# Kernel tuning notes

Measured on AMD Instinct MI355X. Metric: run time of the kernel, lower is better.

Reference implementation:

```python
import jax, jax.numpy as jnp
import numpy as np
import math

B, S, D, H = 2, 2048, 512, 8
DH = D // H  # 64

def setup_inputs() -> dict:
    key = jax.random.key(0)
    ks = jax.random.split(key, 7)
    x = jax.random.normal(ks[0], (B, S, D), jnp.float32)
    shift = jax.random.normal(ks[1], (B, S, S), jnp.float32)
    mask = jax.random.randint(ks[2], (B, S, S), 0, 2).astype(jnp.float32)
    W = jax.random.normal(ks[3], (3 * D, D), jnp.float32) / math.sqrt(D)
    b = jnp.zeros((3 * D,), jnp.float32)
    Wo = jax.random.normal(ks[4], (D, D), jnp.float32) / math.sqrt(D)
    bo = jnp.zeros((D,), jnp.float32)
    return {"x": x, "shift": shift, "mask": mask, "W": W, "b": b, "Wo": Wo, "bo": bo}

def reference(x, shift, mask, W, b, Wo, bo):
    # qkv projection: (B,S,3D). torch chunk(n_heads) then chunk(3) =>
    # per-head layout is [q_h | k_h | v_h] within each 3*DH-sized slice.
    qkv = x @ W.T + b
    qkv = qkv.reshape(B, S, H, 3, DH)
    qkv = jnp.moveaxis(qkv, (2, 3), (0, 1))  # (H, 3, B, S, DH)
    q, k, v = qkv[:, 0], qkv[:, 1], qkv[:, 2]  # each (H, B, S, DH)

    head_scale = jnp.exp2(-jnp.arange(H, dtype=jnp.float32)).reshape(H, 1, 1, 1)  # 2^-h
    logits = jnp.einsum('hbqd,hbkd->hbqk', q, k) / math.sqrt(DH)
    logits = logits - head_scale * shift[None]          # ALiBi-style per-head shift
    m = mask[None]                                       # (1,B,S,S)
    logits = logits * m - 1e8 * (1.0 - m)
    att = jax.nn.softmax(logits, axis=-1)
    o = jnp.einsum('hbqk,hbkd->hbqd', att, v)            # (H,B,S,DH)
    o = jnp.moveaxis(o, 0, 2).reshape(B, S, D)           # concat heads on last dim
    return o @ Wo.T + bo
```

## Files before the change

### kernel.cpp

```cpp
#include <hip/hip_runtime.h>
#include <math.h>

constexpr int Bc = 2, Sc = 2048, Dc = 512, Hc = 8, DHc = 64;
constexpr int NQKV = 3 * Dc;

typedef unsigned short u16;
typedef unsigned int u32;
typedef __attribute__((ext_vector_type(8))) __bf16 bf16x8;
typedef __attribute__((ext_vector_type(16))) float f32x16;

#define MFMA32 __builtin_amdgcn_mfma_f32_32x32x16_bf16

__device__ inline uint2 splitpack2(float a, float b) {
  u32 ua = __float_as_uint(a), ub = __float_as_uint(b);
  u32 hi = (ub & 0xFFFF0000u) | (ua >> 16);
  float ra = a - __uint_as_float(ua & 0xFFFF0000u);
  float rb = b - __uint_as_float(ub & 0xFFFF0000u);
  u32 lo = (__float_as_uint(rb) & 0xFFFF0000u) | (__float_as_uint(ra) >> 16);
  return uint2{hi, lo};
}
__device__ inline void split1(float v, u16& hi, u16& lo) {
  u32 u = __float_as_uint(v);
  hi = (u16)(u >> 16);
  float r = v - __uint_as_float(u & 0xFFFF0000u);
  lo = (u16)(__float_as_uint(r) >> 16);
}

__global__ __launch_bounds__(256) void presplit_xw(
    const float* __restrict__ x, const float* __restrict__ W,
    u16* __restrict__ Xhi, u16* __restrict__ Xlo, u16* __restrict__ Whi,
    u16* __restrict__ Wlo) {
  const u32 g = blockIdx.x * 256 + threadIdx.x;
  const float* src;
  u16 *dh, *dl;
  if (g < 262144u) {
    src = x + (size_t)g * 8;
    dh = Xhi + (size_t)g * 8;
    dl = Xlo + (size_t)g * 8;
  } else {
    const u32 gw = g - 262144u;
    src = W + (size_t)gw * 8;
    dh = Whi + (size_t)gw * 8;
    dl = Wlo + (size_t)gw * 8;
  }
  const float4 v0 = *(const float4*)src;
  const float4 v1 = *(const float4*)(src + 4);
  const uint2 p0 = splitpack2(v0.x, v0.y), p1 = splitpack2(v0.z, v0.w);
  const uint2 p2 = splitpack2(v1.x, v1.y), p3 = splitpack2(v1.z, v1.w);
  *(uint4*)dh = uint4{p0.x, p1.x, p2.x, p3.x};
  *(uint4*)dl = uint4{p0.y, p1.y, p2.y, p3.y};
}

__global__ __launch_bounds__(256) void presplit_wo(const float* __restrict__ Wo,
                                                   u16* __restrict__ Wohi,
                                                   u16* __restrict__ Wolo) {
  const u32 g = blockIdx.x * 256 + threadIdx.x;
  const float* src = Wo + (size_t)g * 8;
  const float4 v0 = *(const float4*)src;
  const float4 v1 = *(const float4*)(src + 4);
  const uint2 p0 = splitpack2(v0.x, v0.y), p1 = splitpack2(v0.z, v0.w);
  const uint2 p2 = splitpack2(v1.x, v1.y), p3 = splitpack2(v1.z, v1.w);
  *(uint4*)(Wohi + (size_t)g * 8) = uint4{p0.x, p1.x, p2.x, p3.x};
  *(uint4*)(Wolo + (size_t)g * 8) = uint4{p0.y, p1.y, p2.y, p3.y};
}

#define G1_ISSUE(K0)                          \
  {                                           \
    a0h = *(const uint4*)(srcA0h + (K0));     \
    a0l = *(const uint4*)(srcA0l + (K0));     \
    a1h = *(const uint4*)(srcA1h + (K0));     \
    a1l = *(const uint4*)(srcA1l + (K0));     \
    b0h = *(const uint4*)(srcBh + (K0));      \
    b0l = *(const uint4*)(srcBl + (K0));      \
  }
#define G1_COMMIT()                           \
  {                                           \
    *(uint4*)dA0h = a0h;                      \
    *(uint4*)dA0l = a0l;                      \
    *(uint4*)dA1h = a1h;                      \
    *(uint4*)dA1l = a1l;                      \
    *(uint4*)dBh = b0h;                       \
    *(uint4*)dBl = b0l;                       \
  }

__global__ __launch_bounds__(256, 3) void gemm1_mfma(
    const u16* __restrict__ Xhi, const u16* __restrict__ Xlo,
    const u16* __restrict__ Whi, const u16* __restrict__ Wlo,
    const float* __restrict__ bias, u16* __restrict__ Qhi,
    u16* __restrict__ Qlo, u16* __restrict__ Khi, u16* __restrict__ Klo,
    u16* __restrict__ Vthi, u16* __restrict__ Vtlo) {
  __shared__ __align__(16) u16 pool[18432];
  const int tid = threadIdx.x;
  const int wave = tid >> 6, lane = tid & 63, l31 = lane & 31, lhi = lane >> 5;
  const int wm = wave >> 1, wn = wave & 1;
  const int m0 = blockIdx.y * 128, n0 = blockIdx.x * 64;

  const int mA = tid >> 2, kgA = tid & 3;
  const int rowA = (kgA & 1) * 32 + (mA & 31);
  u16* const dA0h = &pool[(((mA >> 5) * 2 + (kgA >> 1)) * 64 + rowA) * 8];
  u16* const dA0l = dA0h + 4096;
  u16* const dA1h =
      &pool[(((2 + (mA >> 5)) * 2 + (kgA >> 1)) * 64 + rowA) * 8];
  u16* const dA1l = dA1h + 4096;
  u16* const dBh = &pool[8192 + (((mA >> 5) * 2 + (kgA >> 1)) * 64 + rowA) * 8];
  u16* const dBl = dBh + 2048;
  const u16* const srcA0h = Xhi + (size_t)(m0 + mA) * 512 + kgA * 8;
  const u16* const srcA0l = Xlo + (size_t)(m0 + mA) * 512 + kgA * 8;
  const u16* const srcA1h = srcA0h + 64 * 512;
  const u16* const srcA1l = srcA0l + 64 * 512;
  const u16* const srcBh = Whi + (size_t)(n0 + mA) * 512 + kgA * 8;
  const u16* const srcBl = Wlo + (size_t)(n0 + mA) * 512 + kgA * 8;

  f32x16 acc[2];
#pragma unroll
  for (int r = 0; r < 16; ++r) {
    acc[0][r] = 0.f;
    acc[1][r] = 0.f;
  }

  uint4 a0h, a0l, a1h, a1l, b0h, b0l;
  G1_ISSUE(0);
  for (int k0 = 0; k0 < 512; k0 += 32) {
    G1_COMMIT();
    __syncthreads();
    if (k0 < 480) G1_ISSUE(k0 + 32);
#pragma unroll
    for (int t = 0; t < 2; ++t) {
      const bf16x8 bh =
          *(const bf16x8*)&pool[8192 + (((0 * 2 + wn) * 2 + t) * 64 + lane) * 8];
      const bf16x8 bl =
          *(const bf16x8*)&pool[8192 + (((1 * 2 + wn) * 2 + t) * 64 + lane) * 8];
#pragma unroll
      for (int ti = 0; ti < 2; ++ti) {
        const bf16x8 ah =
            *(const bf16x8*)&pool[(((0 * 4 + wm * 2 + ti) * 2 + t) * 64 + lane) * 8];
        const bf16x8 al =
            *(const bf16x8*)&pool[(((1 * 4 + wm * 2 + ti) * 2 + t) * 64 + lane) * 8];
        acc[ti] = MFMA32(ah, bh, acc[ti], 0, 0, 0);
        acc[ti] = MFMA32(ah, bl, acc[ti], 0, 0, 0);
        acc[ti] = MFMA32(al, bh, acc[ti], 0, 0, 0);
      }
    }
    __syncthreads();
  }

  const int n = n0 + wn * 32 + l31;
  const float bn = bias[n];
  const int h = n0 / 192;
  const int t3 = (n0 % 192) / 64;
  const int dh = wn * 32 + l31;
  const int batch = m0 >> 11;
  const int s0 = m0 & 2047;
  const int hbq = h * 2 + batch;

#pragma unroll
  for (int ti = 0; ti < 2; ++ti)
#pragma unroll
    for (int r = 0; r < 16; ++r) {
      const int tl = wm * 64 + ti * 32 + (r & 3) + 8 * (r >> 2) + 4 * lhi;
      float val = acc[ti][r] + bn;
      if (t3 == 0) val *= 0.125f;
      u16 hi, lo;
      split1(val, hi, lo);
      pool[tl * 72 + dh] = hi;
      pool[9216 + tl * 72 + dh] = lo;
    }
  __syncthreads();

  u16 *d0, *d1;
  if (t3 == 0) {
    d0 = Qhi;
    d1 = Qlo;
  } else if (t3 == 1) {
    d0 = Khi;
    d1 = Klo;
  } else {
    d0 = Vthi;
    d1 = Vtlo;
  }

  if (t3 != 2) {
    const size_t base = ((size_t)hbq * 2048 + s0) * 64;
#pragma unroll
    for (int p = 0; p < 2; ++p) {
      u16* dst = (p ? d1 : d0) + base;
#pragma unroll
      for (int j = 0; j < 4; ++j) {
        const int g = tid * 32 + j * 8;
        const int token = g >> 6, dh8 = g & 63;
        *(uint4*)(dst + g) = *(const uint4*)&pool[p * 9216 + token * 72 + dh8];
      }
    }
  } else {
    const int d = tid >> 2, tp = (tid & 3) * 32;
#pragma unroll
    for (int p = 0; p < 2; ++p) {
      u16* dst = (p ? d1 : d0) + ((size_t)hbq * 64 + d) * 2048 + s0 + tp;
      u32 w[16];
#pragma unroll
      for (int j = 0; j < 16; ++j) {
        const u16 a = pool[p * 9216 + (tp + 2 * j) * 72 + d];
        const u16 b2 = pool[p * 9216 + (tp + 2 * j + 1) * 72 + d];
        w[j] = (u32)a | ((u32)b2 << 16);
      }
#pragma unroll
      for (int j = 0; j < 4; ++j)
        *(uint4*)(dst + j * 8) =
            uint4{w[4 * j], w[4 * j + 1], w[4 * j + 2], w[4 * j + 3]};
    }
  }
}

constexpr int KF0 = 8320;
constexpr int VF0 = 16512;
constexpr int PF0 = 24704;

#define ISSUE_TILE(KT)                                   \
  {                                                      \
    const float* sp_ = shr + (KT);                       \
    const float* mp_ = mkr + (KT);                       \
    pS0 = *(const float4*)(sp_);                         \
    pS1 = *(const float4*)(sp_ + 4);                     \
    pS2 = *(const float4*)(sp_ + 8);                     \
    pS3 = *(const float4*)(sp_ + 12);                    \
    pM0 = *(const float4*)(mp_);                         \
    pM1 = *(const float4*)(mp_ + 4);                     \
    pM2 = *(const float4*)(mp_ + 8);                     \
    pM3 = *(const float4*)(mp_ + 12);                    \
    const u16* h_ = kvsrc_hi + (size_t)(KT) * ktmul;     \
    const u16* l_ = kvsrc_lo + (size_t)(KT) * ktmul;     \
    pK0 = *(const uint4*)(h_);                           \
    pK1 = *(const uint4*)(l_);                           \
    pK2 = *(const uint4*)(h_ + 8);                       \
    pK3 = *(const uint4*)(l_ + 8);                       \
    pK4 = *(const uint4*)(h_ + 16);                      \
    pK5 = *(const uint4*)(l_ + 16);                      \
    pK6 = *(const uint4*)(h_ + 24);                      \
    pK7 = *(const uint4*)(l_ + 24);                      \
  }

#define COMMIT_TILE()                                    \
  {                                                      \
    smd[0 * 65] = (pM0.x != 0.f) ? pS0.x : 1e13f;        \
    smd[1 * 65] = (pM0.y != 0.f) ? pS0.y : 1e13f;        \
    smd[2 * 65] = (pM0.z != 0.f) ? pS0.z : 1e13f;        \
    smd[3 * 65] = (pM0.w != 0.f) ? pS0.w : 1e13f;        \
    smd[4 * 65] = (pM1.x != 0.f) ? pS1.x : 1e13f;        \
    smd[5 * 65] = (pM1.y != 0.f) ? pS1.y : 1e13f;        \
    smd[6 * 65] = (pM1.z != 0.f) ? pS1.z : 1e13f;        \
    smd[7 * 65] = (pM1.w != 0.f) ? pS1.w : 1e13f;        \
    smd[8 * 65] = (pM2.x != 0.f) ? pS2.x : 1e13f;        \
    smd[9 * 65] = (pM2.y != 0.f) ? pS2.y : 1e13f;        \
    smd[10 * 65] = (pM2.z != 0.f) ? pS2.z : 1e13f;       \
    smd[11 * 65] = (pM2.w != 0.f) ? pS2.w : 1e13f;       \
    smd[12 * 65] = (pM3.x != 0.f) ? pS3.x : 1e13f;       \
    smd[13 * 65] = (pM3.y != 0.f) ? pS3.y : 1e13f;       \
    smd[14 * 65] = (pM3.z != 0.f) ? pS3.z : 1e13f;       \
    smd[15 * 65] = (pM3.w != 0.f) ? pS3.w : 1e13f;       \
    *(uint4*)(kvdst + 0) = pK0;                          \
    *(uint4*)(kvdst + 4096) = pK1;                       \
    *(uint4*)(kvdst + 256) = pK2;                        \
    *(uint4*)(kvdst + 4096 + 256) = pK3;                 \
    *(uint4*)(kvdst + 512) = pK4;                        \
    *(uint4*)(kvdst + 4096 + 512) = pK5;                 \
    *(uint4*)(kvdst + 768) = pK6;                        \
    *(uint4*)(kvdst + 4096 + 768) = pK7;                 \
  }

__global__ __launch_bounds__(256, 2) void attn_mfma(
    const u16* __restrict__ Qhi, const u16* __restrict__ Qlo,
    const u16* __restrict__ Khi, const u16* __restrict__ Klo,
    const u16* __restrict__ Vthi, const u16* __restrict__ Vtlo,
    const float* __restrict__ shift, const float* __restrict__ mask,
    u16* __restrict__ Othi, u16* __restrict__ Otlo) {
  const int head = blockIdx.z, b = blockIdx.y, qb = blockIdx.x;
  const int tid = threadIdx.x;
  const int wave = tid >> 6;
  const int wq = wave >> 1, wk = wave & 1;
  const int lane = tid & 63;
  const int l31 = lane & 31, lhi = lane >> 5;

  __shared__ __align__(16) u16 smem[32896];
  float* SMs = (float*)smem;
  u16* Pw = smem + PF0 + wave * 2048;

  const size_t hb = (size_t)head * Bc + b;
  const int ql = wq * 32 + l31;
  const int qg = qb * 64 + ql;

  bf16x8 qf[2][4];
  {
    const size_t qbase = (hb * Sc + qg) * DHc;
#pragma unroll
    for (int t = 0; t < 4; ++t) {
      qf[0][t] = *(const bf16x8*)(Qhi + qbase + t * 16 + lhi * 8);
      qf[1][t] = *(const bf16x8*)(Qlo + qbase + t * 16 + lhi * 8);
    }
  }
  const float hs = exp2f(-(float)head);

  const int smq = tid >> 2, smk = (tid & 3) * 16;
  const float* shr = shift + ((size_t)b * Sc + qb * 64 + smq) * Sc + smk;
  const float* mkr = mask + ((size_t)b * Sc + qb * 64 + smq) * Sc + smk;
  float* const smd = SMs + (size_t)smk * 65 + smq;

  const int kr = lane >> 1, kh2 = lane & 1;
  const size_t kfix = (hb * Sc + wk * 32 + kr) * 64 + kh2 * 32;
  const size_t vfix = (hb * 64 + lane) * 2048 + wk * 32;
  const int vmt = lane >> 5, vdl = lane & 31;

  const u16* const kvsrc_hi = (wq == 0) ? (Khi + kfix) : (Vthi + vfix);
  const u16* const kvsrc_lo = (wq == 0) ? (Klo + kfix) : (Vtlo + vfix);
  const int ktmul = (wq == 0) ? 64 : 1;
  u16* const kvdst = (wq == 0)
                         ? &smem[KF0 + (wk * 4 + kh2 * 2) * 512 + kr * 8]
                         : &smem[VF0 + (wk * 4 + vmt * 2) * 512 + vdl * 8];

  float m_run = -INFINITY, l_run = 0.f;
  f32x16 o0, o1;
#pragma unroll
  for (int i = 0; i < 16; ++i) {
    o0[i] = 0.f;
    o1[i] = 0.f;
  }

  float4 pS0, pS1, pS2, pS3, pM0, pM1, pM2, pM3;
  uint4 pK0, pK1, pK2, pK3, pK4, pK5, pK6, pK7;

  ISSUE_TILE(0);
  for (int it = 0; it < 32; ++it) {
    COMMIT_TILE();
    __syncthreads();
    if (it < 31) ISSUE_TILE(it * 64 + 64);

    f32x16 s;
#pragma unroll
    for (int i = 0; i < 16; ++i) s[i] = 0.f;
    __builtin_amdgcn_s_setprio(1);
#pragma unroll
    for (int t = 0; t < 4; ++t) {
      const bf16x8 kh = *(const bf16x8*)&smem[KF0 +
          (((0 * 2 + wk) * 4 + t) * 64 + lane) * 8];
      const bf16x8 kl = *(const bf16x8*)&smem[KF0 +
          (((1 * 2 + wk) * 4 + t) * 64 + lane) * 8];
      s = MFMA32(kh, qf[0][t], s, 0, 0, 0);
      s = MFMA32(kh, qf[1][t], s, 0, 0, 0);
      s = MFMA32(kl, qf[0][t], s, 0, 0, 0);
    }
    __builtin_amdgcn_s_setprio(0);

    float p[16];
    float kmax = -INFINITY;
#pragma unroll
    for (int c = 0; c < 4; ++c) {
#pragma unroll
      for (int e = 0; e < 4; ++e) {
        const int kl_ = wk * 32 + c * 8 + lhi * 4 + e;
        const float a = hs * SMs[(size_t)kl_ * 65 + ql];
        const float lg = s[4 * c + e] - a;
        p[4 * c + e] = lg;
        kmax = fmaxf(kmax, lg);
      }
    }
    kmax = fmaxf(kmax, __shfl_xor(kmax, 32, 64));
    const float mnew = fmaxf(m_run, kmax);
    const float alpha = __expf(m_run - mnew);
    float rsum = 0.f;
#pragma unroll
    for (int r = 0; r < 16; ++r) {
      p[r] = __expf(p[r] - mnew);
      rsum += p[r];
    }
    rsum += __shfl_xor(rsum, 32, 64);
    l_run = l_run * alpha + rsum;
    m_run = mnew;
#pragma unroll
    for (int i = 0; i < 16; ++i) {
      o0[i] *= alpha;
      o1[i] *= alpha;
    }

#pragma unroll
    for (int c = 0; c < 4; ++c) {
      const uint2 s01 = splitpack2(p[4 * c + 0], p[4 * c + 1]);
      const uint2 s23 = splitpack2(p[4 * c + 2], p[4 * c + 3]);
      const int t = c >> 1, lh = c & 1;
      const int bi = (t * 64 + lh * 32 + l31) * 8 + lhi * 4;
      *(uint2*)&Pw[bi] = uint2{s01.x, s23.x};
      *(uint2*)&Pw[1024 + bi] = uint2{s01.y, s23.y};
    }

    __builtin_amdgcn_s_setprio(1);
#pragma unroll
    for (int t = 0; t < 2; ++t) {
      const bf16x8 ph = *(const bf16x8*)&Pw[(t * 64 + lane) * 8];
      const bf16x8 pl_ = *(const bf16x8*)&Pw[1024 + (t * 64 + lane) * 8];
      bf16x8 vh = *(const bf16x8*)&smem[VF0 +
          ((((0 * 2 + wk) * 2 + 0) * 2 + t) * 64 + lane) * 8];
      bf16x8 vl = *(const bf16x8*)&smem[VF0 +
          ((((1 * 2 + wk) * 2 + 0) * 2 + t) * 64 + lane) * 8];
      o0 = MFMA32(vh, ph, o0, 0, 0, 0);
      o0 = MFMA32(vh, pl_, o0, 0, 0, 0);
      o0 = MFMA32(vl, ph, o0, 0, 0, 0);
      vh = *(const bf16x8*)&smem[VF0 +
          ((((0 * 2 + wk) * 2 + 1) * 2 + t) * 64 + lane) * 8];
      vl = *(const bf16x8*)&smem[VF0 +
          ((((1 * 2 + wk) * 2 + 1) * 2 + t) * 64 + lane) * 8];
      o1 = MFMA32(vh, ph, o1, 0, 0, 0);
      o1 = MFMA32(vh, pl_, o1, 0, 0, 0);
      o1 = MFMA32(vl, ph, o1, 0, 0, 0);
    }
    __builtin_amdgcn_s_setprio(0);
    __syncthreads();
  }

  float* mL = (float*)(smem + KF0);
  float* lL = mL + 64;
  float* Om = lL + 64;
  if (wk == 1) {
    if (lhi == 0) {
      mL[wq * 32 + l31] = m_run;
      lL[wq * 32 + l31] = l_run;
    }
#pragma unroll
    for (int mt = 0; mt < 2; ++mt)
#pragma unroll
      for (int r = 0; r < 16; ++r) {
        const int row = mt * 32 + (r & 3) + 8 * (r >> 2) + 4 * lhi;
        Om[(wq * 64 + row) * 33 + l31] = (mt ? o1[r] : o0[r]);
      }
  }
  __syncthreads();
  if (wk == 0) {
    const float m1 = mL[wq * 32 + l31];
    const float l1v = lL[wq * 32 + l31];
    const float mst = fmaxf(m_run, m1);
    const float a0 = __expf(m_run - mst), a1 = __expf(m1 - mst);
    const float inv = 1.f / (a0 * l_run + a1 * l1v);
    const int tok = b * 2048 + qg;
#pragma unroll
    for (int mt = 0; mt < 2; ++mt)
#pragma unroll
      for (int r = 0; r < 16; ++r) {
        const int row = mt * 32 + (r & 3) + 8 * (r >> 2) + 4 * lhi;
        const float val = (a0 * (mt ? o1[r] : o0[r]) +
                           a1 * Om[(wq * 64 + row) * 33 + l31]) *
                          inv;
        const int d = head * 64 + row;
        u16 hi, lo;
        split1(val, hi, lo);
        const size_t idx = ((size_t)(d >> 3) * 4096 + tok) * 8 + (d & 7);
        Othi[idx] = hi;
        Otlo[idx] = lo;
      }
  }
}

#define G2_ISSUE(K0)                                        \
  {                                                         \
    g2ah = *(const uint4*)(srcAh + (size_t)(K0) * 4096);    \
    g2al = *(const uint4*)(srcAl + (size_t)(K0) * 4096);    \
    g2bh = *(const uint4*)(srcBh + (K0));                   \
    g2bl = *(const uint4*)(srcBl + (K0));                   \
  }
#define G2_COMMIT()                                         \
  {                                                         \
    *(uint4*)dAh = g2ah;                                    \
    *(uint4*)dAl = g2al;                                    \
    *(uint4*)dBh = g2bh;                                    \
    *(uint4*)dBl = g2bl;                                    \
  }

__global__ __launch_bounds__(256, 2) void gemm2_mfma(
    const u16* __restrict__ Othi, const u16* __restrict__ Otlo,
    const u16* __restrict__ Wohi, const u16* __restrict__ Wolo,
    const float* __restrict__ bo, float* __restrict__ out) {
  __shared__ __align__(16) u16 Af[2][2][2][64][8];
  __shared__ __align__(16) u16 Bf[2][2][2][64][8];
  const int tid = threadIdx.x;
  const int wave = tid >> 6, lane = tid & 63, l31 = lane & 31, lhi = lane >> 5;
  const int wm = wave >> 1, wn = wave & 1;
  const int m0 = blockIdx.y * 64, n0 = blockIdx.x * 64;

  const int cA = tid >> 6, tokA = tid & 63;
  u16* const dAh = &Af[0][tokA >> 5][cA >> 1][(cA & 1) * 32 + (tokA & 31)][0];
  u16* const dAl = &Af[1][tokA >> 5][cA >> 1][(cA & 1) * 32 + (tokA & 31)][0];
  const u16* const srcAh = Othi + ((size_t)cA * 4096 + m0 + tokA) * 8;
  const u16* const srcAl = Otlo + ((size_t)cA * 4096 + m0 + tokA) * 8;
  const int nB = tid >> 2, cB = tid & 3;
  u16* const dBh = &Bf[0][nB >> 5][cB >> 1][(cB & 1) * 32 + (nB & 31)][0];
  u16* const dBl = &Bf[1][nB >> 5][cB >> 1][(cB & 1) * 32 + (nB & 31)][0];
  const u16* const srcBh = Wohi + (size_t)(n0 + nB) * 512 + cB * 8;
  const u16* const srcBl = Wolo + (size_t)(n0 + nB) * 512 + cB * 8;

  f32x16 acc;
#pragma unroll
  for (int r = 0; r < 16; ++r) acc[r] = 0.f;

  uint4 g2ah, g2al, g2bh, g2bl;
  G2_ISSUE(0);
  for (int k0 = 0; k0 < 512; k0 += 32) {
    G2_COMMIT();
    __syncthreads();
    if (k0 < 480) G2_ISSUE(k0 + 32);
#pragma unroll
    for (int t = 0; t < 2; ++t) {
      const bf16x8 ah = *(const bf16x8*)&Af[0][wm][t][lane][0];
      const bf16x8 al = *(const bf16x8*)&Af[1][wm][t][lane][0];
      const bf16x8 bh = *(const bf16x8*)&Bf[0][wn][t][lane][0];
      const bf16x8 bl = *(const bf16x8*)&Bf[1][wn][t][lane][0];
      acc = MFMA32(ah, bh, acc, 0, 0, 0);
      acc = MFMA32(ah, bl, acc, 0, 0, 0);
      acc = MFMA32(al, bh, acc, 0, 0, 0);
    }
    __syncthreads();
  }

  const int n = n0 + wn * 32 + l31;
  const float bn = bo[n];
#pragma unroll
  for (int r = 0; r < 16; ++r) {
    const int m = m0 + wm * 32 + (r & 3) + 8 * (r >> 2) + 4 * lhi;
    out[(size_t)m * 512 + n] = acc[r] + bn;
  }
}

extern "C" void kernel_launch(void* const* d_in, const int* in_sizes, int n_in,
                              void* d_out, int out_size, void* d_ws,
                              size_t ws_size, hipStream_t stream) {
  const float* x = (const float*)d_in[0];
  const float* shift = (const float*)d_in[1];
  const float* mask = (const float*)d_in[2];
  const float* W = (const float*)d_in[3];
  const float* b = (const float*)d_in[4];
  const float* Wo = (const float*)d_in[5];
  const float* bo = (const float*)d_in[6];
  float* out = (float*)d_out;

  const size_t P = (size_t)Hc * Bc * Sc * DHc;
  u16* ws0 = (u16*)d_ws;
  u16* Qhi = ws0;
  u16* Qlo = ws0 + P;
  u16* Khi = ws0 + 2 * P;
  u16* Klo = ws0 + 3 * P;
  u16* Vthi = ws0 + 4 * P;
  u16* Vtlo = ws0 + 5 * P;
  u16* Othi = ws0 + 6 * P;
  u16* Otlo = ws0 + 7 * P;
  u16* Xhi = ws0 + 6 * P;
  u16* Xlo = ws0 + 7 * P;
  u16* Whi = (u16*)out;
  u16* Wlo = (u16*)out + 786432;
  u16* Wohi = ws0;
  u16* Wolo = ws0 + 262144;

  presplit_xw<<<dim3(1408), 256, 0, stream>>>(x, W, Xhi, Xlo, Whi, Wlo);

  gemm1_mfma<<<dim3(NQKV / 64, (Bc * Sc) / 128), 256, 0, stream>>>(
      Xhi, Xlo, Whi, Wlo, b, Qhi, Qlo, Khi, Klo, Vthi, Vtlo);

  attn_mfma<<<dim3(Sc / 64, Bc, Hc), 256, 0, stream>>>(
      Qhi, Qlo, Khi, Klo, Vthi, Vtlo, shift, mask, Othi, Otlo);

  presplit_wo<<<dim3(128), 256, 0, stream>>>(Wo, Wohi, Wolo);

  gemm2_mfma<<<dim3(Dc / 64, (Bc * Sc) / 64), 256, 0, stream>>>(
      Othi, Otlo, Wohi, Wolo, bo, out);
}
```

Before: 252.5 us.

## Deepen gemm1 K-tile to 64 and swizzle block order for XCD locality

```diff
diff --git a/kernel.cpp b/kernel.cpp
--- a/kernel.cpp
+++ b/kernel.cpp
@@ -64,23 +64,35 @@
   *(uint4*)(Wolo + (size_t)g * 8) = uint4{p0.y, p1.y, p2.y, p3.y};
 }
 
-#define G1_ISSUE(K0)                          \
-  {                                           \
-    a0h = *(const uint4*)(srcA0h + (K0));     \
-    a0l = *(const uint4*)(srcA0l + (K0));     \
-    a1h = *(const uint4*)(srcA1h + (K0));     \
-    a1l = *(const uint4*)(srcA1l + (K0));     \
-    b0h = *(const uint4*)(srcBh + (K0));      \
-    b0l = *(const uint4*)(srcBl + (K0));      \
-  }
-#define G1_COMMIT()                           \
-  {                                           \
-    *(uint4*)dA0h = a0h;                      \
-    *(uint4*)dA0l = a0l;                      \
-    *(uint4*)dA1h = a1h;                      \
-    *(uint4*)dA1l = a1l;                      \
-    *(uint4*)dBh = b0h;                       \
-    *(uint4*)dBl = b0l;                       \
+#define G1_ISSUE(K0)                              \
+  {                                               \
+    pa0h = *(const uint4*)(srcAh + (K0));         \
+    pa0l = *(const uint4*)(srcAl + (K0));         \
+    pa1h = *(const uint4*)(srcAh + 16384 + (K0)); \
+    pa1l = *(const uint4*)(srcAl + 16384 + (K0)); \
+    pa2h = *(const uint4*)(srcAh + 32768 + (K0)); \
+    pa2l = *(const uint4*)(srcAl + 32768 + (K0)); \
+    pa3h = *(const uint4*)(srcAh + 49152 + (K0)); \
+    pa3l = *(const uint4*)(srcAl + 49152 + (K0)); \
+    pb0h = *(const uint4*)(srcBh + (K0));         \
+    pb0l = *(const uint4*)(srcBl + (K0));         \
+    pb1h = *(const uint4*)(srcBh + 16384 + (K0)); \
+    pb1l = *(const uint4*)(srcBl + 16384 + (K0)); \
+  }
+#define G1_COMMIT()                 \
+  {                                 \
+    *(uint4*)(dA + 0) = pa0h;       \
+    *(uint4*)(dA + 8192) = pa0l;    \
+    *(uint4*)(dA + 2048) = pa1h;    \
+    *(uint4*)(dA + 10240) = pa1l;   \
+    *(uint4*)(dA + 4096) = pa2h;    \
+    *(uint4*)(dA + 12288) = pa2l;   \
+    *(uint4*)(dA + 6144) = pa3h;    \
+    *(uint4*)(dA + 14336) = pa3l;   \
+    *(uint4*)(dB + 0) = pb0h;       \
+    *(uint4*)(dB + 4096) = pb0l;    \
+    *(uint4*)(dB + 2048) = pb1h;    \
+    *(uint4*)(dB + 6144) = pb1l;    \
   }
 
 __global__ __launch_bounds__(256, 3) void gemm1_mfma(
@@ -89,27 +101,23 @@
     const float* __restrict__ bias, u16* __restrict__ Qhi,
     u16* __restrict__ Qlo, u16* __restrict__ Khi, u16* __restrict__ Klo,
     u16* __restrict__ Vthi, u16* __restrict__ Vtlo) {
-  __shared__ __align__(16) u16 pool[18432];
+  __shared__ __align__(16) u16 pool[24576];
   const int tid = threadIdx.x;
   const int wave = tid >> 6, lane = tid & 63, l31 = lane & 31, lhi = lane >> 5;
   const int wm = wave >> 1, wn = wave & 1;
-  const int m0 = blockIdx.y * 128, n0 = blockIdx.x * 64;
-
-  const int mA = tid >> 2, kgA = tid & 3;
-  const int rowA = (kgA & 1) * 32 + (mA & 31);
-  u16* const dA0h = &pool[(((mA >> 5) * 2 + (kgA >> 1)) * 64 + rowA) * 8];
-  u16* const dA0l = dA0h + 4096;
-  u16* const dA1h =
-      &pool[(((2 + (mA >> 5)) * 2 + (kgA >> 1)) * 64 + rowA) * 8];
-  u16* const dA1l = dA1h + 4096;
-  u16* const dBh = &pool[8192 + (((mA >> 5) * 2 + (kgA >> 1)) * 64 + rowA) * 8];
-  u16* const dBl = dBh + 2048;
-  const u16* const srcA0h = Xhi + (size_t)(m0 + mA) * 512 + kgA * 8;
-  const u16* const srcA0l = Xlo + (size_t)(m0 + mA) * 512 + kgA * 8;
-  const u16* const srcA1h = srcA0h + 64 * 512;
-  const u16* const srcA1l = srcA0l + 64 * 512;
-  const u16* const srcBh = Whi + (size_t)(n0 + mA) * 512 + kgA * 8;
-  const u16* const srcBl = Wlo + (size_t)(n0 + mA) * 512 + kgA * 8;
+  const u32 wg = blockIdx.x;
+  const u32 swz = (wg & 7) * 96 + (wg >> 3);
+  const int n0 = (swz % 24) * 64, m0 = (swz / 24) * 128;
+
+  const int mr = tid >> 3, kg = tid & 7;
+  const int ksub = kg >> 1;
+  const int rowA = (kg & 1) * 32 + mr;
+  u16* const dA = &pool[ksub * 512 + rowA * 8];
+  u16* const dB = &pool[16384 + ksub * 512 + rowA * 8];
+  const u16* const srcAh = Xhi + (size_t)(m0 + mr) * 512 + kg * 8;
+  const u16* const srcAl = Xlo + (size_t)(m0 + mr) * 512 + kg * 8;
+  const u16* const srcBh = Whi + (size_t)(n0 + mr) * 512 + kg * 8;
+  const u16* const srcBl = Wlo + (size_t)(n0 + mr) * 512 + kg * 8;
 
   f32x16 acc[2];
 #pragma unroll
@@ -118,24 +126,25 @@
     acc[1][r] = 0.f;
   }
 
-  uint4 a0h, a0l, a1h, a1l, b0h, b0l;
+  uint4 pa0h, pa0l, pa1h, pa1l, pa2h, pa2l, pa3h, pa3l;
+  uint4 pb0h, pb0l, pb1h, pb1l;
   G1_ISSUE(0);
-  for (int k0 = 0; k0 < 512; k0 += 32) {
+  for (int k0 = 0; k0 < 512; k0 += 64) {
     G1_COMMIT();
     __syncthreads();
-    if (k0 < 480) G1_ISSUE(k0 + 32);
-#pragma unroll
-    for (int t = 0; t < 2; ++t) {
+    if (k0 < 448) G1_ISSUE(k0 + 64);
+#pragma unroll
+    for (int t = 0; t < 4; ++t) {
       const bf16x8 bh =
-          *(const bf16x8*)&pool[8192 + (((0 * 2 + wn) * 2 + t) * 64 + lane) * 8];
+          *(const bf16x8*)&pool[16384 + ((0 * 2 + wn) * 4 + t) * 512 + lane * 8];
       const bf16x8 bl =
-          *(const bf16x8*)&pool[8192 + (((1 * 2 + wn) * 2 + t) * 64 + lane) * 8];
+          *(const bf16x8*)&pool[16384 + ((1 * 2 + wn) * 4 + t) * 512 + lane * 8];
 #pragma unroll
       for (int ti = 0; ti < 2; ++ti) {
         const bf16x8 ah =
-            *(const bf16x8*)&pool[(((0 * 4 + wm * 2 + ti) * 2 + t) * 64 + lane) * 8];
+            *(const bf16x8*)&pool[((0 * 4 + wm * 2 + ti) * 4 + t) * 512 + lane * 8];
         const bf16x8 al =
-            *(const bf16x8*)&pool[(((1 * 4 + wm * 2 + ti) * 2 + t) * 64 + lane) * 8];
+            *(const bf16x8*)&pool[((1 * 4 + wm * 2 + ti) * 4 + t) * 512 + lane * 8];
         acc[ti] = MFMA32(ah, bh, acc[ti], 0, 0, 0);
         acc[ti] = MFMA32(ah, bl, acc[ti], 0, 0, 0);
         acc[ti] = MFMA32(al, bh, acc[ti], 0, 0, 0);
@@ -480,7 +489,9 @@
   const int tid = threadIdx.x;
   const int wave = tid >> 6, lane = tid & 63, l31 = lane & 31, lhi = lane >> 5;
   const int wm = wave >> 1, wn = wave & 1;
-  const int m0 = blockIdx.y * 64, n0 = blockIdx.x * 64;
+  const u32 wg = blockIdx.x;
+  const u32 swz = (wg & 7) * 64 + (wg >> 3);
+  const int n0 = (swz % 8) * 64, m0 = (swz / 8) * 64;
 
   const int cA = tid >> 6, tokA = tid & 63;
   u16* const dAh = &Af[0][tokA >> 5][cA >> 1][(cA & 1) * 32 + (tokA & 31)][0];
@@ -556,14 +567,13 @@
 
   presplit_xw<<<dim3(1408), 256, 0, stream>>>(x, W, Xhi, Xlo, Whi, Wlo);
 
-  gemm1_mfma<<<dim3(NQKV / 64, (Bc * Sc) / 128), 256, 0, stream>>>(
-      Xhi, Xlo, Whi, Wlo, b, Qhi, Qlo, Khi, Klo, Vthi, Vtlo);
+  gemm1_mfma<<<dim3(768), 256, 0, stream>>>(Xhi, Xlo, Whi, Wlo, b, Qhi, Qlo,
+                                            Khi, Klo, Vthi, Vtlo);
 
   attn_mfma<<<dim3(Sc / 64, Bc, Hc), 256, 0, stream>>>(
       Qhi, Qlo, Khi, Klo, Vthi, Vtlo, shift, mask, Othi, Otlo);
 
   presplit_wo<<<dim3(128), 256, 0, stream>>>(Wo, Wohi, Wolo);
 
-  gemm2_mfma<<<dim3(Dc / 64, (Bc * Sc) / 64), 256, 0, stream>>>(
-      Othi, Otlo, Wohi, Wolo, bo, out);
-}
+  gemm2_mfma<<<dim3(512), 256, 0, stream>>>(Othi, Otlo, Wohi, Wolo, bo, out);
+}
```

Result: slower. 260.0 us (+2.9%).
